# Optimization experiments

Hardware: AMD Instinct MI355X
Metric: run time of the kernel (lower is better)

The kernel has to match this reference:

```python
import jax, jax.numpy as jnp
import numpy as np

D_MODEL = 1024
N_HEADS = 16
D_KV = 64
N_CONTEXT = 20
PASSAGE_LEN = 200
BSZ = 8
QLEN = 32
KLEN = N_CONTEXT * PASSAGE_LEN


def setup_inputs() -> dict:
    key = jax.random.key(0)
    ks = jax.random.split(key, 8)
    inp = {
        "input": jax.random.normal(ks[0], (BSZ, QLEN, D_MODEL), jnp.float32),
        "kv": jax.random.normal(ks[1], (BSZ, KLEN, D_MODEL), jnp.float32),
        "mask_add": jnp.zeros((BSZ, 1, 1, KLEN), jnp.float32),
        "mask_bool": jnp.ones((BSZ, 1, 1, KLEN), bool),
        "position_bias": jax.random.normal(ks[2], (1, N_HEADS, QLEN, KLEN), jnp.float32),
        "Wq": jax.random.normal(ks[3], (D_MODEL, N_HEADS * D_KV), jnp.float32) * 0.02,
        "Wk": jax.random.normal(ks[4], (D_MODEL, N_HEADS * D_KV), jnp.float32) * 0.02,
        "Wv": jax.random.normal(ks[5], (D_MODEL, N_HEADS * D_KV), jnp.float32) * 0.02,
        "Wo": jax.random.normal(ks[6], (N_HEADS * D_KV, D_MODEL), jnp.float32) * 0.02,
        "n_context": N_CONTEXT,
    }
    return inp


def reference(input, kv, mask_add, mask_bool, position_bias, Wq, Wk, Wv, Wo, n_context):
    b, qlen, dm = input.shape
    klen = kv.shape[1]
    H = position_bias.shape[1]
    dh = Wq.shape[1] // H
    # projections, [b, h, len, dh]
    q = (input @ Wq).reshape(b, qlen, H, dh).transpose(0, 2, 1, 3)
    k = (kv @ Wk).reshape(b, klen, H, dh).transpose(0, 2, 1, 3)
    v = (kv @ Wv).reshape(b, klen, H, dh).transpose(0, 2, 1, 3)
    # unscaled T5-style attention scores + additive mask + position bias
    scores = jnp.einsum('bhqd,bhkd->bhqk', q, k) + mask_add + position_bias
    attn = jax.nn.softmax(scores.astype(jnp.float32), axis=-1).astype(scores.dtype)
    # dropout p=0 (eval) -> identity
    out = jnp.einsum('bhqk,bhkd->bhqd', attn, v)
    out = out.transpose(0, 2, 1, 3).reshape(b, qlen, H * dh) @ Wo
    # collect_cross_attention(sum_over_tokens=True): masked avg of raw scores per context
    s = scores.reshape(b, H, qlen, n_context, -1)
    m = mask_bool.reshape(b, 1, 1, n_context, -1).astype(scores.dtype)
    collected = (s * m).sum(-1) / m.sum(-1)  # [b, H, qlen, n_context]
    return out, collected
```

## Files before the change

kernel.cpp:

```cpp
#include <hip/hip_runtime.h>
#include <stdint.h>

constexpr int DMODEL = 1024;
constexpr int NH     = 16;
constexpr int DHD    = 64;
constexpr int BS     = 8;
constexpr int QLEN   = 32;
constexpr int KLEN   = 4000;
constexpr int NCTX   = 20;
constexpr int PLEN   = 200;

typedef __bf16 bf16_t;
typedef bf16_t bf16x8 __attribute__((ext_vector_type(8)));
typedef float  f32x4  __attribute__((ext_vector_type(4)));

__device__ __forceinline__ uint16_t f2bf(float f) {
  uint32_t u = __float_as_uint(f);
  u += 0x7FFF + ((u >> 16) & 1);
  return (uint16_t)(u >> 16);
}

#define GLOAD_LDS16(gsrc, ldst) \
  __builtin_amdgcn_global_load_lds((const __attribute__((address_space(1))) void*)(gsrc), \
                                   (__attribute__((address_space(3))) void*)(ldst), 16, 0, 0)

__global__ void detect_mask(const uint32_t* __restrict__ m, int* __restrict__ flag) {
  if (threadIdx.x == 0 && blockIdx.x == 0)
    *flag = (m[0] == 0x01010101u) ? 1 : 0;
}

__global__ void cast_inputs(const float* __restrict__ kv, const float* __restrict__ inp,
                            uint16_t* __restrict__ kv16, uint16_t* __restrict__ in16) {
  const int NKV4 = (BS * KLEN * DMODEL) / 4;
  const int NIN4 = (BS * QLEN * DMODEL) / 4;
  const int total = NKV4 + NIN4;
  for (int i = blockIdx.x * blockDim.x + threadIdx.x; i < total; i += gridDim.x * blockDim.x) {
    float4 v; uint16_t* dst; int di;
    if (i < NKV4) { v = ((const float4*)kv)[i]; dst = kv16; di = i; }
    else          { v = ((const float4*)inp)[i - NKV4]; dst = in16; di = i - NKV4; }
    ushort4 o; o.x = f2bf(v.x); o.y = f2bf(v.y); o.z = f2bf(v.z); o.w = f2bf(v.w);
    ((ushort4*)dst)[di] = o;
  }
}

__global__ void wtrans(const float* __restrict__ w0, const float* __restrict__ w1,
                       const float* __restrict__ w2, const float* __restrict__ w3,
                       uint16_t* __restrict__ out) {
  __shared__ uint16_t sm[64][65];
  const float* W = (blockIdx.z == 0) ? w0 : (blockIdx.z == 1) ? w1 : (blockIdx.z == 2) ? w2 : w3;
  uint16_t* o = out + (size_t)blockIdx.z * DMODEL * DMODEL;
  int k0 = blockIdx.y * 64, n0 = blockIdx.x * 64;
  int t = threadIdx.x;
  for (int i = 0; i < 16; ++i) {
    int s = t + i * 256; int r = s >> 6, c = s & 63;
    sm[r][c] = f2bf(W[(size_t)(k0 + r) * DMODEL + n0 + c]);
  }
  __syncthreads();
  for (int i = 0; i < 16; ++i) {
    int s = t + i * 256; int r = s >> 6, c = s & 63;
    o[(size_t)(n0 + r) * DMODEL + k0 + c] = sm[c][r];
  }
}

template <int OUT_F32>
__global__ void __launch_bounds__(256) gemm_bt(const uint16_t* __restrict__ A,
                                               const uint16_t* __restrict__ Bt,
                                               void* __restrict__ Cv,
                                               int M, int N, int K) {
  __shared__ __align__(16) uint16_t As[128 * 32];
  __shared__ __align__(16) uint16_t Bs[128 * 32];
  const int m0 = blockIdx.x * 128, n0 = blockIdx.y * 128;
  const int tid = threadIdx.x, lane = tid & 63, wave = tid >> 6;
  const int wm = wave >> 1, wn = wave & 1;
  const int l15 = lane & 15, g = lane >> 4;
  const int sr = lane >> 2, sc = (lane & 3) * 8;
  const int c0 = wave * 2, c1 = wave * 2 + 1;
  f32x4 acc[4][4] = {};
  const int KT = K / 32;
  for (int kt = 0; kt < KT; ++kt) {
    __syncthreads();
    GLOAD_LDS16(A  + (size_t)(m0 + c0 * 16 + sr) * K + kt * 32 + sc, As + c0 * 512);
    GLOAD_LDS16(A  + (size_t)(m0 + c1 * 16 + sr) * K + kt * 32 + sc, As + c1 * 512);
    GLOAD_LDS16(Bt + (size_t)(n0 + c0 * 16 + sr) * K + kt * 32 + sc, Bs + c0 * 512);
    GLOAD_LDS16(Bt + (size_t)(n0 + c1 * 16 + sr) * K + kt * 32 + sc, Bs + c1 * 512);
    __syncthreads();
    bf16x8 a[4], b[4];
#pragma unroll
    for (int i = 0; i < 4; ++i)
      a[i] = *(const bf16x8*)&As[(wm * 64 + i * 16 + l15) * 32 + g * 8];
#pragma unroll
    for (int j = 0; j < 4; ++j)
      b[j] = *(const bf16x8*)&Bs[(wn * 64 + j * 16 + l15) * 32 + g * 8];
#pragma unroll
    for (int i = 0; i < 4; ++i)
#pragma unroll
      for (int j = 0; j < 4; ++j)
        acc[i][j] = __builtin_amdgcn_mfma_f32_16x16x32_bf16(a[i], b[j], acc[i][j], 0, 0, 0);
  }
#pragma unroll
  for (int i = 0; i < 4; ++i)
#pragma unroll
    for (int j = 0; j < 4; ++j) {
      int row = m0 + wm * 64 + i * 16 + g * 4;
      int col = n0 + wn * 64 + j * 16 + l15;
      if (OUT_F32) {
        float* C = (float*)Cv;
#pragma unroll
        for (int r = 0; r < 4; ++r) C[(size_t)(row + r) * N + col] = acc[i][j][r];
      } else {
        uint16_t* C = (uint16_t*)Cv;
#pragma unroll
        for (int r = 0; r < 4; ++r) C[(size_t)(row + r) * N + col] = f2bf(acc[i][j][r]);
      }
    }
}

__global__ void __launch_bounds__(256) gemm_kv(const uint16_t* __restrict__ A,
                                               const uint16_t* __restrict__ Bt,
                                               uint16_t* __restrict__ kmat,
                                               uint16_t* __restrict__ vt) {
  __shared__ __align__(16) uint16_t smem[16384];
  const int orig = blockIdx.x;
  const int swz  = (orig & 7) * 500 + (orig >> 3);
  const int mb = swz >> 4, nb = swz & 15;
  const int m0 = mb * 128, n0 = nb * 128;
  const int tid = threadIdx.x, lane = tid & 63, wave = tid >> 6;
  const int wm = wave >> 1, wn = wave & 1;
  const int l15 = lane & 15, g = lane >> 4;
  const int sr = lane >> 2, sc = (lane & 3) * 8;
  const int c0 = wave * 2, c1 = c0 + 1;
  f32x4 acc[4][4] = {};

#define AS(c) (smem + (c) * 4096)
#define BS_(c) (smem + 8192 + (c) * 4096)
#define STAGE(c, kt)                                                                     \
  do {                                                                                   \
    GLOAD_LDS16(A  + (size_t)(m0 + c0 * 16 + sr) * 1024 + (kt) * 32 + sc, AS(c)  + c0 * 512); \
    GLOAD_LDS16(A  + (size_t)(m0 + c1 * 16 + sr) * 1024 + (kt) * 32 + sc, AS(c)  + c1 * 512); \
    GLOAD_LDS16(Bt + (size_t)(n0 + c0 * 16 + sr) * 1024 + (kt) * 32 + sc, BS_(c) + c0 * 512); \
    GLOAD_LDS16(Bt + (size_t)(n0 + c1 * 16 + sr) * 1024 + (kt) * 32 + sc, BS_(c) + c1 * 512); \
  } while (0)

  STAGE(0, 0);
  __syncthreads();
  int cur = 0;
  for (int kt = 0; kt < 32; ++kt) {
    if (kt < 31) STAGE(cur ^ 1, kt + 1);
    bf16x8 a[4], b[4];
#pragma unroll
    for (int i = 0; i < 4; ++i)
      a[i] = *(const bf16x8*)&AS(cur)[(wm * 64 + i * 16 + l15) * 32 + g * 8];
#pragma unroll
    for (int j = 0; j < 4; ++j)
      b[j] = *(const bf16x8*)&BS_(cur)[(wn * 64 + j * 16 + l15) * 32 + g * 8];
#pragma unroll
    for (int i = 0; i < 4; ++i)
#pragma unroll
      for (int j = 0; j < 4; ++j)
        acc[i][j] = __builtin_amdgcn_mfma_f32_16x16x32_bf16(a[i], b[j], acc[i][j], 0, 0, 0);
    __syncthreads();
    cur ^= 1;
  }
#undef STAGE
#undef BS_
#undef AS

  if (n0 < 1024) {
#pragma unroll
    for (int i = 0; i < 4; ++i)
#pragma unroll
      for (int j = 0; j < 4; ++j) {
        int row = m0 + wm * 64 + i * 16 + g * 4;
        int col = n0 + wn * 64 + j * 16 + l15;
#pragma unroll
        for (int r = 0; r < 4; ++r)
          kmat[(size_t)(row + r) * 1024 + col] = f2bf(acc[i][j][r]);
      }
  } else {
#pragma unroll
    for (int i = 0; i < 4; ++i)
#pragma unroll
      for (int j = 0; j < 4; ++j) {
        int dd = wn * 64 + j * 16 + l15;
        int kk = wm * 64 + i * 16 + g * 4;
#pragma unroll
        for (int r = 0; r < 4; ++r)
          smem[dd * 128 + kk + r] = f2bf(acc[i][j][r]);
      }
    __syncthreads();
    const int hbase = (n0 - 1024) >> 6;
#pragma unroll
    for (int it = 0; it < 8; ++it) {
      int s = it * 256 + tid;
      int dd = s >> 4, kk0 = (s & 15) * 8;
      int grow = m0 + kk0;
      int b = grow / 4000, krel = grow - b * 4000;
      int h = hbase + (dd >> 6), d = dd & 63;
      ulonglong2 v = *(const ulonglong2*)&smem[dd * 128 + kk0];
      *(ulonglong2*)&vt[(((size_t)(b * NH + h) * DHD + d) * KLEN) + krel] = v;
    }
  }
}

__global__ void __launch_bounds__(256) fused_attn(const uint16_t* __restrict__ Q,
                                                  const uint16_t* __restrict__ Km,
                                                  const uint16_t* __restrict__ Vt,
                                                  const float* __restrict__ mask_add,
                                                  const void* __restrict__ maskb,
                                                  const int* __restrict__ flag,
                                                  const float* __restrict__ bias,
                                                  float* __restrict__ part,
                                                  float* __restrict__ coll) {
  __shared__ __align__(16) uint16_t plds[4][32 * 32];
  const int kc = blockIdx.x, h = blockIdx.y, b = blockIdx.z;
  const int lane = threadIdx.x & 63, wave = threadIdx.x >> 6;
  const int l15 = lane & 15, g = lane >> 4;
  const int ctx = kc * 4 + wave;
  const int kbase = ctx * PLEN;
  const int fm = *flag;

  bf16x8 aq[2][2];
#pragma unroll
  for (int i = 0; i < 2; ++i)
#pragma unroll
    for (int ks = 0; ks < 2; ++ks)
      aq[i][ks] = *(const bf16x8*)&Q[(size_t)(b * QLEN + i * 16 + l15) * DMODEL + h * DHD + ks * 32 + g * 8];

  f32x4 o[2][4] = {};
  float mr[2][4], lr[2][4], cs[2][4];
#pragma unroll
  for (int i = 0; i < 2; ++i)
#pragma unroll
    for (int r = 0; r < 4; ++r) { mr[i][r] = -3e38f; lr[i][r] = 0.f; cs[i][r] = 0.f; }
  float cnt = 0.f;

  for (int t = 0; t < 7; ++t) {
    const int k0 = kbase + t * 32;
    bf16x8 kb[2][2];
#pragma unroll
    for (int j = 0; j < 2; ++j) {
      int kr = k0 + j * 16 + l15; if (kr > KLEN - 1) kr = KLEN - 1;
#pragma unroll
      for (int ks = 0; ks < 2; ++ks)
        kb[j][ks] = *(const bf16x8*)&Km[(size_t)(b * KLEN + kr) * DMODEL + h * DHD + ks * 32 + g * 8];
    }
    f32x4 sa[2][2] = {};
#pragma unroll
    for (int ks = 0; ks < 2; ++ks)
#pragma unroll
      for (int i = 0; i < 2; ++i)
#pragma unroll
        for (int j = 0; j < 2; ++j)
          sa[i][j] = __builtin_amdgcn_mfma_f32_16x16x32_bf16(aq[i][ks], kb[j][ks], sa[i][j], 0, 0, 0);

    int colc[2]; bool vd[2], vm[2]; float ma[2];
#pragma unroll
    for (int j = 0; j < 2; ++j) {
      int col = k0 + j * 16 + l15;
      vd[j] = (col < kbase + PLEN);
      int cc = col; if (cc > KLEN - 1) cc = KLEN - 1;
      colc[j] = cc;
      ma[j] = mask_add[b * KLEN + cc];
      bool mk = fm ? (((const uint8_t*)maskb)[b * KLEN + cc] != 0)
                   : (((const int*)maskb)[b * KLEN + cc] != 0);
      vm[j] = vd[j] && mk;
    }

    float sv[2][2][4];
    float tmax[2][4];
#pragma unroll
    for (int i = 0; i < 2; ++i)
#pragma unroll
      for (int r = 0; r < 4; ++r) {
        tmax[i][r] = -3e38f;
        const int q = i * 16 + g * 4 + r;
        const size_t brow = (size_t)(h * QLEN + q) * KLEN;
#pragma unroll
        for (int j = 0; j < 2; ++j) {
          float raw = sa[i][j][r] + ma[j] + bias[brow + colc[j]];
          cs[i][r] += vm[j] ? raw : 0.f;
          float x = vd[j] ? raw : -3e38f;
          sv[i][j][r] = x;
          tmax[i][r] = fmaxf(tmax[i][r], x);
        }
      }
#pragma unroll
    for (int j = 0; j < 2; ++j) cnt += vm[j] ? 1.f : 0.f;

#pragma unroll
    for (int i = 0; i < 2; ++i)
#pragma unroll
      for (int r = 0; r < 4; ++r) {
        float v = tmax[i][r];
        v = fmaxf(v, __shfl_xor(v, 1)); v = fmaxf(v, __shfl_xor(v, 2));
        v = fmaxf(v, __shfl_xor(v, 4)); v = fmaxf(v, __shfl_xor(v, 8));
        tmax[i][r] = v;
      }
    float scale[2][4];
#pragma unroll
    for (int i = 0; i < 2; ++i)
#pragma unroll
      for (int r = 0; r < 4; ++r) {
        float mn = fmaxf(mr[i][r], tmax[i][r]);
        scale[i][r] = __expf(mr[i][r] - mn);
        mr[i][r] = mn;
        lr[i][r] *= scale[i][r];
      }
#pragma unroll
    for (int i = 0; i < 2; ++i)
#pragma unroll
      for (int j2 = 0; j2 < 4; ++j2)
#pragma unroll
        for (int r = 0; r < 4; ++r)
          o[i][j2][r] *= scale[i][r];
#pragma unroll
    for (int i = 0; i < 2; ++i)
#pragma unroll
      for (int r = 0; r < 4; ++r) {
        const int q = i * 16 + g * 4 + r;
#pragma unroll
        for (int j = 0; j < 2; ++j) {
          float p = __expf(sv[i][j][r] - mr[i][r]);
          lr[i][r] += p;
          plds[wave][q * 32 + j * 16 + l15] = f2bf(p);
        }
      }
    bf16x8 ap[2];
#pragma unroll
    for (int i = 0; i < 2; ++i)
      ap[i] = *(const bf16x8*)&plds[wave][(i * 16 + l15) * 32 + g * 8];
    bf16x8 vb[4];
    int vc = k0 + g * 8; if (vc > KLEN - 8) vc = KLEN - 8;
#pragma unroll
    for (int j2 = 0; j2 < 4; ++j2)
      vb[j2] = *(const bf16x8*)&Vt[((size_t)((b * NH + h) * DHD + j2 * 16 + l15)) * KLEN + vc];
#pragma unroll
    for (int i = 0; i < 2; ++i)
#pragma unroll
      for (int j2 = 0; j2 < 4; ++j2)
        o[i][j2] = __builtin_amdgcn_mfma_f32_16x16x32_bf16(ap[i], vb[j2], o[i][j2], 0, 0, 0);
  }

#pragma unroll
  for (int i = 0; i < 2; ++i)
#pragma unroll
    for (int r = 0; r < 4; ++r) {
      float v = lr[i][r];
      v += __shfl_xor(v, 1); v += __shfl_xor(v, 2); v += __shfl_xor(v, 4); v += __shfl_xor(v, 8);
      lr[i][r] = v;
      float c = cs[i][r];
      c += __shfl_xor(c, 1); c += __shfl_xor(c, 2); c += __shfl_xor(c, 4); c += __shfl_xor(c, 8);
      cs[i][r] = c;
    }
  { float c = cnt; c += __shfl_xor(c, 1); c += __shfl_xor(c, 2); c += __shfl_xor(c, 4); c += __shfl_xor(c, 8); cnt = c; }

  float* pr = part + ((size_t)((b * NH + h) * NCTX + ctx)) * 32 * 72;
#pragma unroll
  for (int i = 0; i < 2; ++i)
#pragma unroll
    for (int j2 = 0; j2 < 4; ++j2)
#pragma unroll
      for (int r = 0; r < 4; ++r)
        pr[(i * 16 + g * 4 + r) * 72 + 8 + j2 * 16 + l15] = o[i][j2][r];
  if (l15 == 0) {
#pragma unroll
    for (int i = 0; i < 2; ++i)
#pragma unroll
      for (int r = 0; r < 4; ++r) {
        int q = i * 16 + g * 4 + r;
        pr[q * 72 + 0] = mr[i][r];
        pr[q * 72 + 1] = lr[i][r];
        coll[(((size_t)(b * NH + h)) * QLEN + q) * NCTX + ctx] = cs[i][r] / cnt;
      }
  }
}

__global__ void __launch_bounds__(256) combine_attn(const float* __restrict__ part,
                                                    uint16_t* __restrict__ ao16) {
  const int t = threadIdx.x;
  const int row = blockIdx.x * 16 + (t >> 4);
  const int ln = t & 15;
  const int bh = row >> 5, q = row & 31;
  const float* p0 = part + ((size_t)bh * 640 + q) * 72;
  float M = -3e38f;
#pragma unroll
  for (int c = 0; c < NCTX; ++c) M = fmaxf(M, p0[(size_t)c * 2304]);
  float Z = 0.f, o0 = 0.f, o1 = 0.f, o2 = 0.f, o3 = 0.f;
  const int d0 = ln * 4;
  for (int c = 0; c < NCTX; ++c) {
    const float* pc = p0 + (size_t)c * 2304;
    float e = __expf(pc[0] - M);
    Z += e * pc[1];
    float4 ov = *(const float4*)&pc[8 + d0];
    o0 += e * ov.x; o1 += e * ov.y; o2 += e * ov.z; o3 += e * ov.w;
  }
  float iz = 1.f / Z;
  const int b = bh >> 4, h = bh & 15;
  ushort4 w; w.x = f2bf(o0 * iz); w.y = f2bf(o1 * iz); w.z = f2bf(o2 * iz); w.w = f2bf(o3 * iz);
  *(ushort4*)&ao16[(size_t)(b * QLEN + q) * DMODEL + h * DHD + d0] = w;
}

extern "C" void kernel_launch(void* const* d_in, const int* in_sizes, int n_in,
                              void* d_out, int out_size, void* d_ws, size_t ws_size,
                              hipStream_t stream) {
  const float* input     = (const float*)d_in[0];
  const float* kv        = (const float*)d_in[1];
  const float* mask_add  = (const float*)d_in[2];
  const void*  mask_bool = d_in[3];
  const float* bias      = (const float*)d_in[4];
  const float* Wq        = (const float*)d_in[5];
  const float* Wk        = (const float*)d_in[6];
  const float* Wv        = (const float*)d_in[7];
  const float* Wo        = (const float*)d_in[8];
  float* out  = (float*)d_out;
  float* coll = out + (size_t)BS * QLEN * DMODEL;

  char* ws = (char*)d_ws;
  size_t off = 0;
  auto alloc = [&](size_t bytes) { char* p = ws + off; off += (bytes + 255) & ~(size_t)255; return p; };
  uint16_t* kv16 = (uint16_t*)alloc((size_t)BS * KLEN * DMODEL * 2);
  uint16_t* in16 = (uint16_t*)alloc((size_t)BS * QLEN * DMODEL * 2);
  uint16_t* wt   = (uint16_t*)alloc((size_t)4 * DMODEL * DMODEL * 2);
  uint16_t* q16  = (uint16_t*)alloc((size_t)BS * QLEN * DMODEL * 2);
  uint16_t* kmat = (uint16_t*)alloc((size_t)BS * KLEN * DMODEL * 2);
  uint16_t* vt   = (uint16_t*)alloc((size_t)BS * KLEN * DMODEL * 2);
  float*    part = (float*)   alloc((size_t)BS * NH * NCTX * 32 * 72 * 4);
  uint16_t* ao16 = (uint16_t*)alloc((size_t)BS * QLEN * DMODEL * 2);
  int*      flag = (int*)alloc(256);

  uint16_t* WqT  = wt;
  uint16_t* WkvT = wt + (size_t)DMODEL * DMODEL;
  uint16_t* WoT  = wt + (size_t)3 * DMODEL * DMODEL;

  detect_mask<<<1, 64, 0, stream>>>((const uint32_t*)mask_bool, flag);
  cast_inputs<<<2048, 256, 0, stream>>>(kv, input, kv16, in16);
  wtrans<<<dim3(16, 16, 4), 256, 0, stream>>>(Wq, Wk, Wv, Wo, wt);
  gemm_bt<0><<<dim3(2, 8), 256, 0, stream>>>(in16, WqT, q16, BS * QLEN, DMODEL, DMODEL);
  gemm_kv<<<4000, 256, 0, stream>>>(kv16, WkvT, kmat, vt);
  fused_attn<<<dim3(5, NH, BS), 256, 0, stream>>>(q16, kmat, vt, mask_add, mask_bool, flag,
                                                  bias, part, coll);
  combine_attn<<<256, 256, 0, stream>>>(part, ao16);
  gemm_bt<1><<<dim3(2, 8), 256, 0, stream>>>(ao16, WoT, out, BS * QLEN, DMODEL, DMODEL);
}
```

Baseline: 357.1 us.

## Enlarge KV projection GEMM tile to 256x256 with swizzled LDS and BK=64

The K/V projection GEMM moves from 128x128 tiles with 256 threads to 256x256 tiles with 512 threads (8 waves, each computing 128x64), with a K-step of 64 and 128KB of double-buffered LDS. LDS columns are XOR-swizzled to avoid bank conflicts, and synchronisation uses explicit vmcnt waits plus raw barriers so the next stage's loads overlap compute. The larger tile raises arithmetic intensity and cuts global/LDS traffic per FLOP. The cost is occupancy: one block per CU, 128 accumulator registers per thread, and only 1000 blocks, which may leave the last wave of blocks unevenly spread across CUs.

```diff
diff --git a/kernel.cpp b/kernel.cpp
--- a/kernel.cpp
+++ b/kernel.cpp
@@ -115,88 +115,108 @@
     }
 }
 
-__global__ void __launch_bounds__(256) gemm_kv(const uint16_t* __restrict__ A,
+__global__ void __launch_bounds__(512) gemm_kv(const uint16_t* __restrict__ A,
                                                const uint16_t* __restrict__ Bt,
                                                uint16_t* __restrict__ kmat,
                                                uint16_t* __restrict__ vt) {
-  __shared__ __align__(16) uint16_t smem[16384];
+  __shared__ __align__(16) uint16_t smem[65536];
   const int orig = blockIdx.x;
-  const int swz  = (orig & 7) * 500 + (orig >> 3);
-  const int mb = swz >> 4, nb = swz & 15;
-  const int m0 = mb * 128, n0 = nb * 128;
-  const int tid = threadIdx.x, lane = tid & 63, wave = tid >> 6;
-  const int wm = wave >> 1, wn = wave & 1;
+  const int swz  = (orig & 7) * 125 + (orig >> 3);
+  const int mb = swz >> 3, nb = swz & 7;
+  const int m0 = mb * 256, n0 = nb * 256;
+  const int tid = threadIdx.x, lane = tid & 63, wid = tid >> 6;
+  const int wm = wid >> 2, wn = wid & 3;
   const int l15 = lane & 15, g = lane >> 4;
-  const int sr = lane >> 2, sc = (lane & 3) * 8;
-  const int c0 = wave * 2, c1 = c0 + 1;
-  f32x4 acc[4][4] = {};
-
-#define AS(c) (smem + (c) * 4096)
-#define BS_(c) (smem + 8192 + (c) * 4096)
-#define STAGE(c, kt)                                                                     \
-  do {                                                                                   \
-    GLOAD_LDS16(A  + (size_t)(m0 + c0 * 16 + sr) * 1024 + (kt) * 32 + sc, AS(c)  + c0 * 512); \
-    GLOAD_LDS16(A  + (size_t)(m0 + c1 * 16 + sr) * 1024 + (kt) * 32 + sc, AS(c)  + c1 * 512); \
-    GLOAD_LDS16(Bt + (size_t)(n0 + c0 * 16 + sr) * 1024 + (kt) * 32 + sc, BS_(c) + c0 * 512); \
-    GLOAD_LDS16(Bt + (size_t)(n0 + c1 * 16 + sr) * 1024 + (kt) * 32 + sc, BS_(c) + c1 * 512); \
-  } while (0)
+  const int l3 = lane >> 3, l7 = lane & 7;
+  const int cg = (l7 ^ (l3 & 7)) * 8;
+
+  f32x4 acc[8][4] = {};
+
+#define ABASE(bf) (smem + (bf) * 32768)
+#define BBASE(bf) (smem + (bf) * 32768 + 16384)
+
+  auto STAGE = [&](int bf, int kt) {
+    const int colg = kt * 64 + cg;
+#pragma unroll
+    for (int ia = 0; ia < 4; ++ia) {
+      const int r0 = wid * 32 + ia * 8;
+      GLOAD_LDS16(A + (size_t)(m0 + r0 + l3) * 1024 + colg, ABASE(bf) + r0 * 64);
+    }
+#pragma unroll
+    for (int ib = 0; ib < 4; ++ib) {
+      const int r0 = wid * 32 + ib * 8;
+      GLOAD_LDS16(Bt + (size_t)(n0 + r0 + l3) * 1024 + colg, BBASE(bf) + r0 * 64);
+    }
+  };
 
   STAGE(0, 0);
-  __syncthreads();
-  int cur = 0;
-  for (int kt = 0; kt < 32; ++kt) {
-    if (kt < 31) STAGE(cur ^ 1, kt + 1);
-    bf16x8 a[4], b[4];
-#pragma unroll
-    for (int i = 0; i < 4; ++i)
-      a[i] = *(const bf16x8*)&AS(cur)[(wm * 64 + i * 16 + l15) * 32 + g * 8];
-#pragma unroll
-    for (int j = 0; j < 4; ++j)
-      b[j] = *(const bf16x8*)&BS_(cur)[(wn * 64 + j * 16 + l15) * 32 + g * 8];
-#pragma unroll
-    for (int i = 0; i < 4; ++i)
-#pragma unroll
-      for (int j = 0; j < 4; ++j)
-        acc[i][j] = __builtin_amdgcn_mfma_f32_16x16x32_bf16(a[i], b[j], acc[i][j], 0, 0, 0);
-    __syncthreads();
-    cur ^= 1;
-  }
-#undef STAGE
-#undef BS_
-#undef AS
+  for (int kt = 0; kt < 16; ++kt) {
+    const int bf = kt & 1;
+    if (kt < 15) {
+      STAGE(bf ^ 1, kt + 1);
+      asm volatile("s_waitcnt vmcnt(8)" ::: "memory");
+    } else {
+      asm volatile("s_waitcnt vmcnt(0)" ::: "memory");
+    }
+    asm volatile("s_barrier" ::: "memory");
+#pragma unroll
+    for (int kk = 0; kk < 2; ++kk) {
+      bf16x8 af[8], bb[4];
+#pragma unroll
+      for (int mi = 0; mi < 8; ++mi) {
+        const int row = wm * 128 + mi * 16 + l15;
+        const int gr = (kk * 4 + g) ^ (row & 7);
+        af[mi] = *(const bf16x8*)&ABASE(bf)[row * 64 + gr * 8];
+      }
+#pragma unroll
+      for (int ni = 0; ni < 4; ++ni) {
+        const int row = wn * 64 + ni * 16 + l15;
+        const int gr = (kk * 4 + g) ^ (row & 7);
+        bb[ni] = *(const bf16x8*)&BBASE(bf)[row * 64 + gr * 8];
+      }
+#pragma unroll
+      for (int mi = 0; mi < 8; ++mi)
+#pragma unroll
+        for (int ni = 0; ni < 4; ++ni)
+          acc[mi][ni] = __builtin_amdgcn_mfma_f32_16x16x32_bf16(af[mi], bb[ni], acc[mi][ni], 0, 0, 0);
+    }
+    asm volatile("s_barrier" ::: "memory");
+  }
+#undef ABASE
+#undef BBASE
 
   if (n0 < 1024) {
 #pragma unroll
-    for (int i = 0; i < 4; ++i)
-#pragma unroll
-      for (int j = 0; j < 4; ++j) {
-        int row = m0 + wm * 64 + i * 16 + g * 4;
-        int col = n0 + wn * 64 + j * 16 + l15;
+    for (int mi = 0; mi < 8; ++mi)
+#pragma unroll
+      for (int ni = 0; ni < 4; ++ni) {
+        const int row = m0 + wm * 128 + mi * 16 + g * 4;
+        const int col = n0 + wn * 64 + ni * 16 + l15;
 #pragma unroll
         for (int r = 0; r < 4; ++r)
-          kmat[(size_t)(row + r) * 1024 + col] = f2bf(acc[i][j][r]);
+          kmat[(size_t)(row + r) * 1024 + col] = f2bf(acc[mi][ni][r]);
       }
   } else {
 #pragma unroll
-    for (int i = 0; i < 4; ++i)
-#pragma unroll
-      for (int j = 0; j < 4; ++j) {
-        int dd = wn * 64 + j * 16 + l15;
-        int kk = wm * 64 + i * 16 + g * 4;
+    for (int mi = 0; mi < 8; ++mi)
+#pragma unroll
+      for (int ni = 0; ni < 4; ++ni) {
+        const int dd = wn * 64 + ni * 16 + l15;
+        const int kk_tok = wm * 128 + mi * 16 + g * 4;
 #pragma unroll
         for (int r = 0; r < 4; ++r)
-          smem[dd * 128 + kk + r] = f2bf(acc[i][j][r]);
+          smem[dd * 256 + kk_tok + r] = f2bf(acc[mi][ni][r]);
       }
     __syncthreads();
     const int hbase = (n0 - 1024) >> 6;
 #pragma unroll
-    for (int it = 0; it < 8; ++it) {
-      int s = it * 256 + tid;
-      int dd = s >> 4, kk0 = (s & 15) * 8;
-      int grow = m0 + kk0;
-      int b = grow / 4000, krel = grow - b * 4000;
-      int h = hbase + (dd >> 6), d = dd & 63;
-      ulonglong2 v = *(const ulonglong2*)&smem[dd * 128 + kk0];
+    for (int it = 0; it < 16; ++it) {
+      const int sp = it * 512 + tid;
+      const int dd = sp >> 5, kk0 = (sp & 31) * 8;
+      const int grow = m0 + kk0;
+      const int b = grow / 4000, krel = grow - b * 4000;
+      const int h = hbase + (dd >> 6), d = dd & 63;
+      ulonglong2 v = *(const ulonglong2*)&smem[dd * 256 + kk0];
       *(ulonglong2*)&vt[(((size_t)(b * NH + h) * DHD + d) * KLEN) + krel] = v;
     }
   }
@@ -436,7 +456,7 @@
   cast_inputs<<<2048, 256, 0, stream>>>(kv, input, kv16, in16);
   wtrans<<<dim3(16, 16, 4), 256, 0, stream>>>(Wq, Wk, Wv, Wo, wt);
   gemm_bt<0><<<dim3(2, 8), 256, 0, stream>>>(in16, WqT, q16, BS * QLEN, DMODEL, DMODEL);
-  gemm_kv<<<4000, 256, 0, stream>>>(kv16, WkvT, kmat, vt);
+  gemm_kv<<<1000, 512, 0, stream>>>(kv16, WkvT, kmat, vt);
   fused_attn<<<dim3(5, NH, BS), 256, 0, stream>>>(q16, kmat, vt, mask_add, mask_bool, flag,
                                                   bias, part, coll);
   combine_attn<<<256, 256, 0, stream>>>(part, ao16);
```

New measurement: 305.3 us. 14.5% less time.
